# Kernel optimization log

Measured on AMD Instinct MI355X. Metric: run time of the kernel, lower is better.

The kernel has to match this reference:

```python
import jax, jax.numpy as jnp
import numpy as np

EPS = 1e-5
HEADS = 4
N_SIDE = 32  # im_h == im_w


def _rel_pos_indices(n):
    idx = np.arange(n)
    xi = np.repeat(idx, n)
    yi = np.tile(idx, n)
    pos = np.stack([xi, yi])                      # [2, n^2]
    d = pos[:, None, :] - pos[:, :, None]          # [2, n^2, n^2]
    d = np.clip(d, -n, n) + (n - 1)
    return d[0], d[1]


def _conv1x1(x, W):
    # x: [b,c,H,W], W: [o,c]
    return jnp.einsum('bchw,oc->bohw', x, W)


def _bn(x, g, b, m, v):
    inv = jax.lax.rsqrt(v + EPS)
    return (x - m[:, None, None]) * (inv * g)[:, None, None] + b[:, None, None]


def setup_inputs() -> dict:
    key = jax.random.key(0)
    ks = jax.random.split(key, 8)
    b, dim, H = 16, 256, N_SIDE
    dim_k, heads, dim_out = 16, HEADS, 256
    dim_v = dim_out // heads
    return {
        'x': jax.random.normal(ks[0], (b, dim, H, H), jnp.float32),
        'Wq': jax.random.normal(ks[1], (dim_k * heads, dim), jnp.float32) * 0.05,
        'Wk': jax.random.normal(ks[2], (dim_k, dim), jnp.float32) * 0.05,
        'Wv': jax.random.normal(ks[3], (dim_v, dim), jnp.float32) * 0.05,
        'gq': jnp.ones((dim_k * heads,), jnp.float32),
        'bq': jnp.zeros((dim_k * heads,), jnp.float32),
        'mq': jax.random.normal(ks[4], (dim_k * heads,), jnp.float32) * 0.1,
        'vq': jax.random.uniform(ks[5], (dim_k * heads,), jnp.float32, 0.5, 1.5),
        'gv': jnp.ones((dim_v,), jnp.float32),
        'bv': jnp.zeros((dim_v,), jnp.float32),
        'mv': jax.random.normal(ks[6], (dim_v,), jnp.float32) * 0.1,
        'vv': jax.random.uniform(ks[7], (dim_v,), jnp.float32, 0.5, 1.5),
        'rel_pos_emb': jax.random.normal(jax.random.fold_in(key, 7), (2 * H - 1, 2 * H - 1, dim_k), jnp.float32) * 0.05,
    }


def reference(x, Wq, Wk, Wv, gq, bq, mq, vq, gv, bv, mv, vv, rel_pos_emb):
    b, c, H, W = x.shape
    heads = HEADS
    m = H * W
    dim_k = Wk.shape[0]
    dim_v = Wv.shape[0]

    Q = _bn(_conv1x1(x, Wq), gq, bq, mq, vq)              # [b, h*k, H, W]
    K = _conv1x1(x, Wk)                                   # [b, k, H, W]
    V = _bn(_conv1x1(x, Wv), gv, bv, mv, vv)              # [b, v, H, W]

    Q = Q.reshape(b, heads, dim_k, m).transpose(0, 1, 3, 2)   # [b, h, m, k]
    K = K.reshape(b, dim_k, m).transpose(0, 2, 1)             # [b, m, k]
    V = V.reshape(b, dim_v, m).transpose(0, 2, 1)             # [b, m, v]

    sK = jax.nn.softmax(K, axis=-1)  # NOTE: source softmaxes over k, not m
    lam_c = jnp.einsum('bmk,bmv->bkv', sK, V)
    content = jnp.einsum('bhnk,bkv->bnhv', Q, lam_c)

    r0, r1 = _rel_pos_indices(H)
    emb = rel_pos_emb[r0, r1]                         # [m, m, k]
    lam_p = jnp.einsum('nmk,bmv->bnkv', emb, V)       # [b, m, k, v]
    position = jnp.einsum('bhnk,bnkv->bnhv', Q, lam_p)

    out = content + position                          # [b, m, h, v]
    return out.reshape(b, H, W, heads * dim_v)
```

## Files before the change

kernel.cpp:

```cpp
#include <hip/hip_runtime.h>
#include <math.h>

namespace {
typedef unsigned short u16;
typedef __attribute__((ext_vector_type(4))) float f32x4;
typedef __attribute__((ext_vector_type(8))) short bf16x8;

constexpr int kB  = 16;
constexpr int kC  = 256;
constexpr int kM  = 1024;

__device__ inline u16 f2b(float f) {
    union { float f; unsigned u; } un; un.f = f;
    unsigned r = un.u + 0x7FFF + ((un.u >> 16) & 1);
    return (u16)(r >> 16);
}
__device__ inline float b2f(u16 u) {
    union { unsigned u; float f; } un; un.u = ((unsigned)u) << 16; return un.f;
}

__global__ __launch_bounds__(256) void k_wpack(
    const float* __restrict__ Wq, const float* __restrict__ Wk,
    const float* __restrict__ Wv,
    const float* __restrict__ gq, const float* __restrict__ bq,
    const float* __restrict__ mq, const float* __restrict__ vq,
    const float* __restrict__ gv, const float* __restrict__ bv,
    const float* __restrict__ mv, const float* __restrict__ vv,
    u16* __restrict__ Wb, float* __restrict__ bb)
{
    const int t = threadIdx.x;
    const int oc = blockIdx.x * 16 + (t >> 4);
    const int c0 = (t & 15) * 16;
    float s, bias;
    const float* wrow;
    if (oc < 64)      { float inv = rsqrtf(vq[oc] + 1e-5f); s = inv * gq[oc]; bias = bq[oc] - mq[oc] * s; wrow = Wq + (size_t)oc * kC; }
    else if (oc < 80) { s = 1.f; bias = 0.f; wrow = Wk + (size_t)(oc - 64) * kC; }
    else              { int i2 = oc - 80; float inv = rsqrtf(vv[i2] + 1e-5f); s = inv * gv[i2]; bias = bv[i2] - mv[i2] * s; wrow = Wv + (size_t)i2 * kC; }
#pragma unroll
    for (int cc = 0; cc < 16; ++cc)
        Wb[(size_t)oc * kC + c0 + cc] = f2b(wrow[c0 + cc] * s);
    if (c0 == 0) bb[oc] = bias;
}

__global__ __launch_bounds__(256) void k_qkv(
    const float* __restrict__ x, const u16* __restrict__ Wb,
    const float* __restrict__ bb,
    u16* __restrict__ Qb, float* __restrict__ Kf, u16* __restrict__ Vb)
{
    __shared__ float Xs[256][64];

    const int b  = blockIdx.y;
    const int m0 = blockIdx.x * 64;
    const int t  = threadIdx.x;
    const int wv = t >> 6, lane = t & 63, li = lane & 15, lg = lane >> 4;
    const int mw = wv * 16;

#pragma unroll
    for (int j = 0; j < 16; ++j) {
        int e = t + 256 * j;
        int c = e >> 4, m4 = (e & 15) * 4;
        float4 xv = *(const float4*)&x[(size_t)(b * kC + c) * kM + m0 + m4];
        *(float4*)&Xs[c][m4] = xv;
    }
    __syncthreads();

    f32x4 acc[9];
#pragma unroll
    for (int i = 0; i < 9; ++i) acc[i] = (f32x4){0.f, 0.f, 0.f, 0.f};

#pragma unroll 2
    for (int ch = 0; ch < 8; ++ch) {
        const int c0 = ch * 32 + lg * 8;
        float xf[8];
#pragma unroll
        for (int j = 0; j < 8; ++j) xf[j] = Xs[c0 + j][mw + li];
        bf16x8 bfr;
#pragma unroll
        for (int j = 0; j < 8; ++j) bfr[j] = (short)f2b(xf[j]);
#pragma unroll
        for (int tl = 0; tl < 9; ++tl) {
            bf16x8 afr = *(const bf16x8*)&Wb[(size_t)(tl * 16 + li) * kC + c0];
            acc[tl] = __builtin_amdgcn_mfma_f32_16x16x32_bf16(afr, bfr, acc[tl], 0, 0, 0);
        }
    }

    const int m = m0 + mw + li;
#pragma unroll
    for (int tl = 0; tl < 9; ++tl) {
        const int ocb = tl * 16 + lg * 4;
        float o[4];
#pragma unroll
        for (int reg = 0; reg < 4; ++reg) o[reg] = acc[tl][reg] + bb[ocb + reg];

        if (tl < 4) {
            u16 pk[4];
#pragma unroll
            for (int reg = 0; reg < 4; ++reg) pk[reg] = f2b(o[reg]);
            u16* qp = Qb + ((size_t)(b * 4 + tl) * kM + m) * 32;
            *(uint2*)&qp[lg * 4]      = *(const uint2*)pk;
            uint2 z; z.x = 0u; z.y = 0u;
            *(uint2*)&qp[16 + lg * 4] = z;
        } else if (tl == 4) {
#pragma unroll
            for (int reg = 0; reg < 4; ++reg)
                Kf[(size_t)(b * 16 + lg * 4 + reg) * kM + m] = o[reg];
        } else {
            const int vb = (tl - 5) * 16 + lg * 4;
#pragma unroll
            for (int reg = 0; reg < 4; ++reg)
                Vb[(size_t)(b * 64 + vb + reg) * kM + m] = f2b(o[reg]);
        }
    }
}

__global__ __launch_bounds__(256) void k_lam(
    const float* __restrict__ Kf, const u16* __restrict__ Vb,
    float* __restrict__ lam_parts)
{
    __shared__ float Ks[16][64];
    __shared__ float Vsh[64][69];

    const int b = blockIdx.y, mb = blockIdx.x;
    const int m0 = mb * 64;
    const int t = threadIdx.x;
    const float* Kc = Kf + (size_t)b * 16 * kM + m0;
    const u16*   Vc = Vb + (size_t)b * 64 * kM + m0;

#pragma unroll
    for (int j = 0; j < 4; ++j) {
        int e = t + 256 * j;
        Ks[e >> 6][e & 63] = Kc[(size_t)(e >> 6) * kM + (e & 63)];
    }
#pragma unroll
    for (int j = 0; j < 16; ++j) {
        int e = t + 256 * j;
        Vsh[e >> 6][e & 63] = b2f(Vc[(size_t)(e >> 6) * kM + (e & 63)]);
    }
    __syncthreads();

    if (t < 64) {
        float vals[16];
        float mx = -1e30f;
#pragma unroll
        for (int k = 0; k < 16; ++k) { vals[k] = Ks[k][t]; mx = fmaxf(mx, vals[k]); }
        float sum = 0.f;
#pragma unroll
        for (int k = 0; k < 16; ++k) { vals[k] = __expf(vals[k] - mx); sum += vals[k]; }
        const float inv = 1.f / sum;
#pragma unroll
        for (int k = 0; k < 16; ++k) Ks[k][t] = vals[k] * inv;
    }
    __syncthreads();

    const int v = t & 63, kq = t >> 6;
    float a[4] = {0.f, 0.f, 0.f, 0.f};
#pragma unroll 4
    for (int mm = 0; mm < 64; ++mm) {
        const float vv_ = Vsh[v][mm];
#pragma unroll
        for (int j = 0; j < 4; ++j) a[j] += Ks[kq * 4 + j][mm] * vv_;
    }
    float* o = lam_parts + (size_t)(mb * kB + b) * 1024;
#pragma unroll
    for (int j = 0; j < 4; ++j) o[(kq * 4 + j) * 64 + v] = a[j];
}

__global__ __launch_bounds__(256) void k_lam2(
    const float* __restrict__ lam_parts, u16* __restrict__ Vl)
{
    __shared__ float lc[1024];
    const int b = blockIdx.x, t = threadIdx.x;
    for (int e = t; e < 1024; e += 256) {
        float s = 0.f;
#pragma unroll
        for (int p = 0; p < 16; ++p) s += lam_parts[(size_t)(p * kB + b) * 1024 + e];
        lc[e] = s;
    }
    __syncthreads();
    for (int e = t; e < 2048; e += 256) {
        int v = e >> 5, k = e & 31;
        Vl[((size_t)b * 64 + v) * 32 + k] = (k < 16) ? f2b(lc[k * 64 + v]) : (u16)0;
    }
}

__global__ __launch_bounds__(256) void k_rpe(
    const float* __restrict__ rpe, u16* __restrict__ rpe_b)
{
    const int dr = blockIdx.x, t = threadIdx.x;
    for (int e = t; e < 2048; e += 256) {
        int dc = e >> 5, k = e & 31;
        float v = (dc < 63 && k < 16) ? rpe[((size_t)dr * 63 + dc) * 16 + k] : 0.f;
        rpe_b[((size_t)dr * 64 + dc) * 32 + k] = f2b(v);
    }
}

__global__ __launch_bounds__(256) void k_attn(
    const u16* __restrict__ Qb, const u16* __restrict__ Vb,
    const u16* __restrict__ rpe_b, const u16* __restrict__ Vl,
    float* __restrict__ out)
{
    __shared__ u16 Rl[64][40];
    __shared__ u16 Vls[64][40];
    __shared__ u16 Sl[4][32][40];

    const int b = blockIdx.y, nrow = blockIdx.x, n0 = nrow * 32;
    const int t = threadIdx.x;
    const int h = t >> 6, lane = t & 63, li = lane & 15, lg = lane >> 4;

    const u16* Qbase = Qb + ((size_t)(b * 4 + h) * kM + n0) * 32;
    bf16x8 qf[2];
    qf[0] = *(const bf16x8*)&Qbase[(size_t)li * 32 + lg * 8];
    qf[1] = *(const bf16x8*)&Qbase[(size_t)(16 + li) * 32 + lg * 8];

    f32x4 acc[2][4];
    const u16* Vlb = Vl + (size_t)b * 64 * 32;
#pragma unroll
    for (int c = 0; c < 4; ++c) {
        bf16x8 cb = *(const bf16x8*)&Vlb[(size_t)(16 * c + li) * 32 + lg * 8];
        f32x4 z = {0.f, 0.f, 0.f, 0.f};
        acc[0][c] = __builtin_amdgcn_mfma_f32_16x16x32_bf16(qf[0], cb, z, 0, 0, 0);
        acc[1][c] = __builtin_amdgcn_mfma_f32_16x16x32_bf16(qf[1], cb, z, 0, 0, 0);
    }

    const int srow = t >> 2, schk = (t & 3) * 8;
    const u16* Vbb = Vb + (size_t)b * 64 * kM;
    u16* Sh = &Sl[h][0][0];

    for (int mrow = 0; mrow < 32; ++mrow) {
        const int dr = mrow - nrow + 31;
        const int mbase = mrow * 32;
        __syncthreads();
        *(bf16x8*)&Rl[srow][schk]  = *(const bf16x8*)&rpe_b[((size_t)dr * 64 + srow) * 32 + schk];
        *(bf16x8*)&Vls[srow][schk] = *(const bf16x8*)&Vbb[(size_t)srow * kM + mbase + schk];
        __syncthreads();

        f32x4 tg[4][2];
#pragma unroll
        for (int g = 0; g < 4; ++g) {
            bf16x8 ra = *(const bf16x8*)&Rl[16 * g + li][lg * 8];
            f32x4 z = {0.f, 0.f, 0.f, 0.f};
            tg[g][0] = __builtin_amdgcn_mfma_f32_16x16x32_bf16(ra, qf[0], z, 0, 0, 0);
            tg[g][1] = __builtin_amdgcn_mfma_f32_16x16x32_bf16(ra, qf[1], z, 0, 0, 0);
        }

#pragma unroll
        for (int g = 0; g < 4; ++g)
#pragma unroll
            for (int r = 0; r < 2; ++r) {
                const int nl = 16 * r + li;
                const int dcb = 16 * g + 4 * lg;
#pragma unroll
                for (int reg = 0; reg < 4; ++reg) {
                    const int ml = dcb + reg + nl - 31;
                    if ((unsigned)ml < 32u) Sh[nl * 40 + ml] = f2b(tg[g][r][reg]);
                }
            }

        bf16x8 vf[4];
#pragma unroll
        for (int c = 0; c < 4; ++c)
            vf[c] = *(const bf16x8*)&Vls[16 * c + li][lg * 8];
#pragma unroll
        for (int r = 0; r < 2; ++r) {
            bf16x8 sa = *(const bf16x8*)&Sh[(size_t)(16 * r + li) * 40 + lg * 8];
#pragma unroll
            for (int c = 0; c < 4; ++c)
                acc[r][c] = __builtin_amdgcn_mfma_f32_16x16x32_bf16(sa, vf[c], acc[r][c], 0, 0, 0);
        }
    }

    float* ob = out + ((size_t)b * kM + n0) * 256 + h * 64;
#pragma unroll
    for (int r = 0; r < 2; ++r)
#pragma unroll
        for (int c = 0; c < 4; ++c)
#pragma unroll
            for (int reg = 0; reg < 4; ++reg)
                ob[(size_t)(16 * r + 4 * lg + reg) * 256 + 16 * c + li] = acc[r][c][reg];
}

}

extern "C" void kernel_launch(void* const* d_in, const int* in_sizes, int n_in,
                              void* d_out, int out_size, void* d_ws, size_t ws_size,
                              hipStream_t stream) {
    const float* x   = (const float*)d_in[0];
    const float* Wq  = (const float*)d_in[1];
    const float* Wk  = (const float*)d_in[2];
    const float* Wv  = (const float*)d_in[3];
    const float* gq  = (const float*)d_in[4];
    const float* bq  = (const float*)d_in[5];
    const float* mq  = (const float*)d_in[6];
    const float* vq  = (const float*)d_in[7];
    const float* gv  = (const float*)d_in[8];
    const float* bv  = (const float*)d_in[9];
    const float* mv  = (const float*)d_in[10];
    const float* vv  = (const float*)d_in[11];
    const float* rpe = (const float*)d_in[12];
    float* out = (float*)d_out;

    float* Kf        = (float*)d_ws;
    float* lam_parts = Kf + (size_t)16 * 16 * 1024;
    float* bbuf      = lam_parts + (size_t)16 * 16 * 1024;
    u16*   Qb        = (u16*)(bbuf + 256);
    u16*   Vb        = Qb + (size_t)16 * 4 * 1024 * 32;
    u16*   Vl        = Vb + (size_t)16 * 64 * 1024;
    u16*   rpe_b     = Vl + (size_t)16 * 64 * 32;
    u16*   Wb        = rpe_b + (size_t)63 * 64 * 32;

    k_wpack<<<9, 256, 0, stream>>>(Wq, Wk, Wv, gq, bq, mq, vq, gv, bv, mv, vv,
                                   Wb, bbuf);
    k_qkv<<<dim3(16, 16), 256, 0, stream>>>(x, Wb, bbuf, Qb, Kf, Vb);
    k_rpe<<<63, 256, 0, stream>>>(rpe, rpe_b);
    k_lam<<<dim3(16, 16), 256, 0, stream>>>(Kf, Vb, lam_parts);
    k_lam2<<<16, 256, 0, stream>>>(lam_parts, Vl);
    k_attn<<<dim3(32, 16), 256, 0, stream>>>(Qb, Vb, rpe_b, Vl, out);
}
```

Measured before the change: 167.1 us.

## Merge prep kernels, fold lambda reduction into attention, prefetch double-row tiles

Merges the weight-pack and rpe-convert kernels into one launch. The lambda_c reduction moves into the attention kernel, which removes k_lam2 and the Vl buffer. The QKV projection now uses 32-column tiles with waves split between Q/K and V outputs, doubling the block count. k_lam loads V with vectorized reads. The attention loop handles two m-rows per iteration and register-prefetches the next tile's rpe and V data, halving barriers at the cost of larger shared memory and a redundant per-block 16-way sum of lam_parts.

```diff
diff --git a/kernel.cpp b/kernel.cpp
--- a/kernel.cpp
+++ b/kernel.cpp
@@ -19,27 +19,38 @@
     union { unsigned u; float f; } un; un.u = ((unsigned)u) << 16; return un.f;
 }
 
-__global__ __launch_bounds__(256) void k_wpack(
+__global__ __launch_bounds__(256) void k_prep(
     const float* __restrict__ Wq, const float* __restrict__ Wk,
     const float* __restrict__ Wv,
     const float* __restrict__ gq, const float* __restrict__ bq,
     const float* __restrict__ mq, const float* __restrict__ vq,
     const float* __restrict__ gv, const float* __restrict__ bv,
     const float* __restrict__ mv, const float* __restrict__ vv,
-    u16* __restrict__ Wb, float* __restrict__ bb)
+    const float* __restrict__ rpe,
+    u16* __restrict__ Wb, float* __restrict__ bb, u16* __restrict__ rpe_b)
 {
+    const int bid = blockIdx.x;
     const int t = threadIdx.x;
-    const int oc = blockIdx.x * 16 + (t >> 4);
-    const int c0 = (t & 15) * 16;
-    float s, bias;
-    const float* wrow;
-    if (oc < 64)      { float inv = rsqrtf(vq[oc] + 1e-5f); s = inv * gq[oc]; bias = bq[oc] - mq[oc] * s; wrow = Wq + (size_t)oc * kC; }
-    else if (oc < 80) { s = 1.f; bias = 0.f; wrow = Wk + (size_t)(oc - 64) * kC; }
-    else              { int i2 = oc - 80; float inv = rsqrtf(vv[i2] + 1e-5f); s = inv * gv[i2]; bias = bv[i2] - mv[i2] * s; wrow = Wv + (size_t)i2 * kC; }
-#pragma unroll
-    for (int cc = 0; cc < 16; ++cc)
-        Wb[(size_t)oc * kC + c0 + cc] = f2b(wrow[c0 + cc] * s);
-    if (c0 == 0) bb[oc] = bias;
+    if (bid < 9) {
+        const int oc = bid * 16 + (t >> 4);
+        const int c0 = (t & 15) * 16;
+        float s, bias;
+        const float* wrow;
+        if (oc < 64)      { float inv = rsqrtf(vq[oc] + 1e-5f); s = inv * gq[oc]; bias = bq[oc] - mq[oc] * s; wrow = Wq + (size_t)oc * kC; }
+        else if (oc < 80) { s = 1.f; bias = 0.f; wrow = Wk + (size_t)(oc - 64) * kC; }
+        else              { int i2 = oc - 80; float inv = rsqrtf(vv[i2] + 1e-5f); s = inv * gv[i2]; bias = bv[i2] - mv[i2] * s; wrow = Wv + (size_t)i2 * kC; }
+#pragma unroll
+        for (int cc = 0; cc < 16; ++cc)
+            Wb[(size_t)oc * kC + c0 + cc] = f2b(wrow[c0 + cc] * s);
+        if (c0 == 0) bb[oc] = bias;
+    } else {
+        const int dr = bid - 9;
+        for (int e = t; e < 2048; e += 256) {
+            int dc = e >> 5, k = e & 31;
+            float v = (dc < 63 && k < 16) ? rpe[((size_t)dr * 63 + dc) * 16 + k] : 0.f;
+            rpe_b[((size_t)dr * 64 + dc) * 32 + k] = f2b(v);
+        }
+    }
 }
 
 __global__ __launch_bounds__(256) void k_qkv(
@@ -47,68 +58,86 @@
     const float* __restrict__ bb,
     u16* __restrict__ Qb, float* __restrict__ Kf, u16* __restrict__ Vb)
 {
-    __shared__ float Xs[256][64];
+    __shared__ float Xs[256][36];
 
     const int b  = blockIdx.y;
-    const int m0 = blockIdx.x * 64;
+    const int m0 = blockIdx.x * 32;
     const int t  = threadIdx.x;
-    const int wv = t >> 6, lane = t & 63, li = lane & 15, lg = lane >> 4;
-    const int mw = wv * 16;
-
-#pragma unroll
-    for (int j = 0; j < 16; ++j) {
+    const int w  = t >> 6, lane = t & 63, li = lane & 15, lg = lane >> 4;
+    const int mh = w & 1, tg = w >> 1;
+    const int mw = mh * 16;
+
+#pragma unroll
+    for (int j = 0; j < 8; ++j) {
         int e = t + 256 * j;
-        int c = e >> 4, m4 = (e & 15) * 4;
-        float4 xv = *(const float4*)&x[(size_t)(b * kC + c) * kM + m0 + m4];
-        *(float4*)&Xs[c][m4] = xv;
+        int c = e >> 3, m4 = (e & 7) * 4;
+        *(float4*)&Xs[c][m4] = *(const float4*)&x[(size_t)(b * kC + c) * kM + m0 + m4];
     }
     __syncthreads();
 
-    f32x4 acc[9];
-#pragma unroll
-    for (int i = 0; i < 9; ++i) acc[i] = (f32x4){0.f, 0.f, 0.f, 0.f};
-
+    const int m = m0 + mw + li;
+
+    if (tg == 0) {
+        f32x4 acc[5];
+#pragma unroll
+        for (int i = 0; i < 5; ++i) acc[i] = (f32x4){0.f, 0.f, 0.f, 0.f};
 #pragma unroll 2
-    for (int ch = 0; ch < 8; ++ch) {
-        const int c0 = ch * 32 + lg * 8;
-        float xf[8];
-#pragma unroll
-        for (int j = 0; j < 8; ++j) xf[j] = Xs[c0 + j][mw + li];
-        bf16x8 bfr;
-#pragma unroll
-        for (int j = 0; j < 8; ++j) bfr[j] = (short)f2b(xf[j]);
-#pragma unroll
-        for (int tl = 0; tl < 9; ++tl) {
-            bf16x8 afr = *(const bf16x8*)&Wb[(size_t)(tl * 16 + li) * kC + c0];
-            acc[tl] = __builtin_amdgcn_mfma_f32_16x16x32_bf16(afr, bfr, acc[tl], 0, 0, 0);
-        }
-    }
-
-    const int m = m0 + mw + li;
-#pragma unroll
-    for (int tl = 0; tl < 9; ++tl) {
-        const int ocb = tl * 16 + lg * 4;
-        float o[4];
-#pragma unroll
-        for (int reg = 0; reg < 4; ++reg) o[reg] = acc[tl][reg] + bb[ocb + reg];
-
-        if (tl < 4) {
-            u16 pk[4];
-#pragma unroll
-            for (int reg = 0; reg < 4; ++reg) pk[reg] = f2b(o[reg]);
-            u16* qp = Qb + ((size_t)(b * 4 + tl) * kM + m) * 32;
-            *(uint2*)&qp[lg * 4]      = *(const uint2*)pk;
-            uint2 z; z.x = 0u; z.y = 0u;
-            *(uint2*)&qp[16 + lg * 4] = z;
-        } else if (tl == 4) {
-#pragma unroll
-            for (int reg = 0; reg < 4; ++reg)
-                Kf[(size_t)(b * 16 + lg * 4 + reg) * kM + m] = o[reg];
-        } else {
-            const int vb = (tl - 5) * 16 + lg * 4;
-#pragma unroll
-            for (int reg = 0; reg < 4; ++reg)
-                Vb[(size_t)(b * 64 + vb + reg) * kM + m] = f2b(o[reg]);
+        for (int ch = 0; ch < 8; ++ch) {
+            const int c0 = ch * 32 + lg * 8;
+            bf16x8 bfr;
+#pragma unroll
+            for (int j = 0; j < 8; ++j) bfr[j] = (short)f2b(Xs[c0 + j][mw + li]);
+#pragma unroll
+            for (int i = 0; i < 5; ++i) {
+                bf16x8 afr = *(const bf16x8*)&Wb[(size_t)(i * 16 + li) * kC + c0];
+                acc[i] = __builtin_amdgcn_mfma_f32_16x16x32_bf16(afr, bfr, acc[i], 0, 0, 0);
+            }
+        }
+#pragma unroll
+        for (int i = 0; i < 5; ++i) {
+            const int ocb = i * 16 + lg * 4;
+            float o[4];
+#pragma unroll
+            for (int reg = 0; reg < 4; ++reg) o[reg] = acc[i][reg] + bb[ocb + reg];
+            if (i < 4) {
+                u16 pk[4];
+#pragma unroll
+                for (int reg = 0; reg < 4; ++reg) pk[reg] = f2b(o[reg]);
+                u16* qp = Qb + ((size_t)(b * 4 + i) * kM + m) * 32;
+                *(uint2*)&qp[lg * 4] = *(const uint2*)pk;
+                uint2 z; z.x = 0u; z.y = 0u;
+                *(uint2*)&qp[16 + lg * 4] = z;
+            } else {
+#pragma unroll
+                for (int reg = 0; reg < 4; ++reg)
+                    Kf[(size_t)(b * 16 + lg * 4 + reg) * kM + m] = o[reg];
+            }
+        }
+    } else {
+        f32x4 acc[4];
+#pragma unroll
+        for (int i = 0; i < 4; ++i) acc[i] = (f32x4){0.f, 0.f, 0.f, 0.f};
+#pragma unroll 2
+        for (int ch = 0; ch < 8; ++ch) {
+            const int c0 = ch * 32 + lg * 8;
+            bf16x8 bfr;
+#pragma unroll
+            for (int j = 0; j < 8; ++j) bfr[j] = (short)f2b(Xs[c0 + j][mw + li]);
+#pragma unroll
+            for (int i = 0; i < 4; ++i) {
+                bf16x8 afr = *(const bf16x8*)&Wb[(size_t)((5 + i) * 16 + li) * kC + c0];
+                acc[i] = __builtin_amdgcn_mfma_f32_16x16x32_bf16(afr, bfr, acc[i], 0, 0, 0);
+            }
+        }
+#pragma unroll
+        for (int i = 0; i < 4; ++i) {
+            const int ocb = (5 + i) * 16 + lg * 4;
+            const int vb = i * 16 + lg * 4;
+#pragma unroll
+            for (int reg = 0; reg < 4; ++reg) {
+                float o = acc[i][reg] + bb[ocb + reg];
+                Vb[(size_t)(b * 64 + vb + reg) * kM + m] = f2b(o);
+            }
         }
     }
 }
@@ -132,9 +161,13 @@
         Ks[e >> 6][e & 63] = Kc[(size_t)(e >> 6) * kM + (e & 63)];
     }
 #pragma unroll
-    for (int j = 0; j < 16; ++j) {
+    for (int j = 0; j < 4; ++j) {
         int e = t + 256 * j;
-        Vsh[e >> 6][e & 63] = b2f(Vc[(size_t)(e >> 6) * kM + (e & 63)]);
+        int v = e >> 4, mq = (e & 15) * 4;
+        uint2 pv = *(const uint2*)&Vc[(size_t)v * kM + mq];
+        u16 pp[4]; *(uint2*)pp = pv;
+#pragma unroll
+        for (int i = 0; i < 4; ++i) Vsh[v][mq + i] = b2f(pp[i]);
     }
     __syncthreads();
 
@@ -165,107 +198,118 @@
     for (int j = 0; j < 4; ++j) o[(kq * 4 + j) * 64 + v] = a[j];
 }
 
-__global__ __launch_bounds__(256) void k_lam2(
-    const float* __restrict__ lam_parts, u16* __restrict__ Vl)
-{
-    __shared__ float lc[1024];
-    const int b = blockIdx.x, t = threadIdx.x;
-    for (int e = t; e < 1024; e += 256) {
-        float s = 0.f;
-#pragma unroll
-        for (int p = 0; p < 16; ++p) s += lam_parts[(size_t)(p * kB + b) * 1024 + e];
-        lc[e] = s;
-    }
-    __syncthreads();
-    for (int e = t; e < 2048; e += 256) {
-        int v = e >> 5, k = e & 31;
-        Vl[((size_t)b * 64 + v) * 32 + k] = (k < 16) ? f2b(lc[k * 64 + v]) : (u16)0;
-    }
-}
-
-__global__ __launch_bounds__(256) void k_rpe(
-    const float* __restrict__ rpe, u16* __restrict__ rpe_b)
-{
-    const int dr = blockIdx.x, t = threadIdx.x;
-    for (int e = t; e < 2048; e += 256) {
-        int dc = e >> 5, k = e & 31;
-        float v = (dc < 63 && k < 16) ? rpe[((size_t)dr * 63 + dc) * 16 + k] : 0.f;
-        rpe_b[((size_t)dr * 64 + dc) * 32 + k] = f2b(v);
-    }
-}
-
 __global__ __launch_bounds__(256) void k_attn(
     const u16* __restrict__ Qb, const u16* __restrict__ Vb,
-    const u16* __restrict__ rpe_b, const u16* __restrict__ Vl,
+    const u16* __restrict__ rpe_b, const float* __restrict__ lam_parts,
     float* __restrict__ out)
 {
-    __shared__ u16 Rl[64][40];
-    __shared__ u16 Vls[64][40];
-    __shared__ u16 Sl[4][32][40];
+    __shared__ u16 Rl[128][40];
+    __shared__ u16 Vls[64][72];
+    __shared__ u16 Sl[4][32][72];
+    __shared__ float lc[16][65];
 
     const int b = blockIdx.y, nrow = blockIdx.x, n0 = nrow * 32;
     const int t = threadIdx.x;
     const int h = t >> 6, lane = t & 63, li = lane & 15, lg = lane >> 4;
+    const u16* Vbb = Vb + (size_t)b * 64 * kM;
+    u16* Sh = &Sl[h][0][0];
+
+    for (int e = t; e < 1024; e += 256) {
+        float s = 0.f;
+#pragma unroll
+        for (int p = 0; p < 16; ++p) s += lam_parts[(size_t)(p * kB + b) * 1024 + e];
+        lc[e >> 6][e & 63] = s;
+    }
 
     const u16* Qbase = Qb + ((size_t)(b * 4 + h) * kM + n0) * 32;
     bf16x8 qf[2];
     qf[0] = *(const bf16x8*)&Qbase[(size_t)li * 32 + lg * 8];
     qf[1] = *(const bf16x8*)&Qbase[(size_t)(16 + li) * 32 + lg * 8];
 
+    bf16x8 rpre[2], vpre[2];
+#pragma unroll
+    for (int ii = 0; ii < 2; ++ii) {
+        int s = 2 * t + ii;
+        int rrow = s >> 2, rkc = (s & 3) * 8;
+        int dr = (rrow >> 6) - nrow + 31;
+        rpre[ii] = *(const bf16x8*)&rpe_b[((size_t)dr * 64 + (rrow & 63)) * 32 + rkc];
+        int v = s >> 3, mc = (s & 7) * 8;
+        vpre[ii] = *(const bf16x8*)&Vbb[(size_t)v * kM + mc];
+    }
+
+    __syncthreads();
+
     f32x4 acc[2][4];
-    const u16* Vlb = Vl + (size_t)b * 64 * 32;
 #pragma unroll
     for (int c = 0; c < 4; ++c) {
-        bf16x8 cb = *(const bf16x8*)&Vlb[(size_t)(16 * c + li) * 32 + lg * 8];
+        bf16x8 cb;
+#pragma unroll
+        for (int j = 0; j < 8; ++j) {
+            int k = lg * 8 + j;
+            cb[j] = (k < 16) ? (short)f2b(lc[k][16 * c + li]) : (short)0;
+        }
         f32x4 z = {0.f, 0.f, 0.f, 0.f};
         acc[0][c] = __builtin_amdgcn_mfma_f32_16x16x32_bf16(qf[0], cb, z, 0, 0, 0);
         acc[1][c] = __builtin_amdgcn_mfma_f32_16x16x32_bf16(qf[1], cb, z, 0, 0, 0);
     }
 
-    const int srow = t >> 2, schk = (t & 3) * 8;
-    const u16* Vbb = Vb + (size_t)b * 64 * kM;
-    u16* Sh = &Sl[h][0][0];
-
-    for (int mrow = 0; mrow < 32; ++mrow) {
-        const int dr = mrow - nrow + 31;
-        const int mbase = mrow * 32;
+    for (int it = 0; it < 16; ++it) {
         __syncthreads();
-        *(bf16x8*)&Rl[srow][schk]  = *(const bf16x8*)&rpe_b[((size_t)dr * 64 + srow) * 32 + schk];
-        *(bf16x8*)&Vls[srow][schk] = *(const bf16x8*)&Vbb[(size_t)srow * kM + mbase + schk];
+#pragma unroll
+        for (int ii = 0; ii < 2; ++ii) {
+            int s = 2 * t + ii;
+            *(bf16x8*)&Rl[s >> 2][(s & 3) * 8] = rpre[ii];
+            *(bf16x8*)&Vls[s >> 3][(s & 7) * 8] = vpre[ii];
+        }
         __syncthreads();
-
-        f32x4 tg[4][2];
-#pragma unroll
-        for (int g = 0; g < 4; ++g) {
-            bf16x8 ra = *(const bf16x8*)&Rl[16 * g + li][lg * 8];
-            f32x4 z = {0.f, 0.f, 0.f, 0.f};
-            tg[g][0] = __builtin_amdgcn_mfma_f32_16x16x32_bf16(ra, qf[0], z, 0, 0, 0);
-            tg[g][1] = __builtin_amdgcn_mfma_f32_16x16x32_bf16(ra, qf[1], z, 0, 0, 0);
-        }
-
-#pragma unroll
-        for (int g = 0; g < 4; ++g)
+        if (it < 15) {
+            const int itn = it + 1;
+#pragma unroll
+            for (int ii = 0; ii < 2; ++ii) {
+                int s = 2 * t + ii;
+                int rrow = s >> 2, rkc = (s & 3) * 8;
+                int dr = 2 * itn + (rrow >> 6) - nrow + 31;
+                rpre[ii] = *(const bf16x8*)&rpe_b[((size_t)dr * 64 + (rrow & 63)) * 32 + rkc];
+                int v = s >> 3, mc = (s & 7) * 8;
+                vpre[ii] = *(const bf16x8*)&Vbb[(size_t)v * kM + itn * 64 + mc];
+            }
+        }
+
+#pragma unroll
+        for (int mi = 0; mi < 2; ++mi) {
+            f32x4 tq[4][2];
+#pragma unroll
+            for (int g = 0; g < 4; ++g) {
+                bf16x8 ra = *(const bf16x8*)&Rl[mi * 64 + 16 * g + li][lg * 8];
+                f32x4 z = {0.f, 0.f, 0.f, 0.f};
+                tq[g][0] = __builtin_amdgcn_mfma_f32_16x16x32_bf16(ra, qf[0], z, 0, 0, 0);
+                tq[g][1] = __builtin_amdgcn_mfma_f32_16x16x32_bf16(ra, qf[1], z, 0, 0, 0);
+            }
+#pragma unroll
+            for (int g = 0; g < 4; ++g)
+#pragma unroll
+                for (int r = 0; r < 2; ++r) {
+                    const int nl = 16 * r + li;
+                    const int dcb = 16 * g + 4 * lg;
+#pragma unroll
+                    for (int reg = 0; reg < 4; ++reg) {
+                        const int ml = dcb + reg + nl - 31;
+                        if ((unsigned)ml < 32u)
+                            Sh[nl * 72 + mi * 32 + ml] = f2b(tq[g][r][reg]);
+                    }
+                }
+
+            bf16x8 vfc[4];
+#pragma unroll
+            for (int c = 0; c < 4; ++c)
+                vfc[c] = *(const bf16x8*)&Vls[16 * c + li][mi * 32 + lg * 8];
 #pragma unroll
             for (int r = 0; r < 2; ++r) {
-                const int nl = 16 * r + li;
-                const int dcb = 16 * g + 4 * lg;
-#pragma unroll
-                for (int reg = 0; reg < 4; ++reg) {
-                    const int ml = dcb + reg + nl - 31;
-                    if ((unsigned)ml < 32u) Sh[nl * 40 + ml] = f2b(tg[g][r][reg]);
-                }
-            }
-
-        bf16x8 vf[4];
-#pragma unroll
-        for (int c = 0; c < 4; ++c)
-            vf[c] = *(const bf16x8*)&Vls[16 * c + li][lg * 8];
-#pragma unroll
-        for (int r = 0; r < 2; ++r) {
-            bf16x8 sa = *(const bf16x8*)&Sh[(size_t)(16 * r + li) * 40 + lg * 8];
-#pragma unroll
-            for (int c = 0; c < 4; ++c)
-                acc[r][c] = __builtin_amdgcn_mfma_f32_16x16x32_bf16(sa, vf[c], acc[r][c], 0, 0, 0);
+                bf16x8 sa = *(const bf16x8*)&Sh[(size_t)(16 * r + li) * 72 + mi * 32 + lg * 8];
+#pragma unroll
+                for (int c = 0; c < 4; ++c)
+                    acc[r][c] = __builtin_amdgcn_mfma_f32_16x16x32_bf16(sa, vfc[c], acc[r][c], 0, 0, 0);
+            }
         }
     }
 
@@ -304,15 +348,12 @@
     float* bbuf      = lam_parts + (size_t)16 * 16 * 1024;
     u16*   Qb        = (u16*)(bbuf + 256);
     u16*   Vb        = Qb + (size_t)16 * 4 * 1024 * 32;
-    u16*   Vl        = Vb + (size_t)16 * 64 * 1024;
-    u16*   rpe_b     = Vl + (size_t)16 * 64 * 32;
+    u16*   rpe_b     = Vb + (size_t)16 * 64 * 1024;
     u16*   Wb        = rpe_b + (size_t)63 * 64 * 32;
 
-    k_wpack<<<9, 256, 0, stream>>>(Wq, Wk, Wv, gq, bq, mq, vq, gv, bv, mv, vv,
-                                   Wb, bbuf);
-    k_qkv<<<dim3(16, 16), 256, 0, stream>>>(x, Wb, bbuf, Qb, Kf, Vb);
-    k_rpe<<<63, 256, 0, stream>>>(rpe, rpe_b);
+    k_prep<<<72, 256, 0, stream>>>(Wq, Wk, Wv, gq, bq, mq, vq, gv, bv, mv, vv,
+                                   rpe, Wb, bbuf, rpe_b);
+    k_qkv<<<dim3(32, 16), 256, 0, stream>>>(x, Wb, bbuf, Qb, Kf, Vb);
     k_lam<<<dim3(16, 16), 256, 0, stream>>>(Kf, Vb, lam_parts);
-    k_lam2<<<16, 256, 0, stream>>>(lam_parts, Vl);
-    k_attn<<<dim3(32, 16), 256, 0, stream>>>(Qb, Vb, rpe_b, Vl, out);
-}
+    k_attn<<<dim3(32, 16), 256, 0, stream>>>(Qb, Vb, rpe_b, lam_parts, out);
+}
```

Measured after the change: 158.3 us. 5.3% less time.
